# Performance work log

Measured on AMD Instinct MI355X. Metric: run time of the kernel, lower is better.

The kernel has to match this reference:

```python
import jax, jax.numpy as jnp
import numpy as np

DIM = 32
N_TOKENS = 4
HIDDEN = 2 * DIM
BATCH = 262144
EPS = 1e-5
SCALE = 1.0 / float(np.sqrt(DIM))


def _ln(x, g, b):
    m = jnp.mean(x, axis=-1, keepdims=True)
    v = jnp.mean((x - m) ** 2, axis=-1, keepdims=True)
    return (x - m) * jax.lax.rsqrt(v + EPS) * g + b


def setup_inputs() -> dict:
    key = jax.random.key(0)
    ks = jax.random.split(key, 16)
    s = 0.02
    lin = lambda k, i, o: jax.random.normal(k, (i, o), jnp.float32) * s
    return {
        "x": jax.random.normal(ks[0], (BATCH, N_TOKENS, DIM), jnp.float32),
        "w_pe": lin(ks[1], DIM, DIM),
        "b_pe": jnp.zeros((DIM,), jnp.float32),
        "pos": jax.random.normal(ks[2], (1, N_TOKENS, DIM), jnp.float32) * s,
        "ln1_g": jnp.ones((DIM,), jnp.float32),
        "ln1_b": jnp.zeros((DIM,), jnp.float32),
        "wq": lin(ks[3], DIM, DIM), "bq": jnp.zeros((DIM,), jnp.float32),
        "wk": lin(ks[4], DIM, DIM), "bk": jnp.zeros((DIM,), jnp.float32),
        "wv": lin(ks[5], DIM, DIM), "bv": jnp.zeros((DIM,), jnp.float32),
        "wo": lin(ks[6], DIM, DIM), "bo": jnp.zeros((DIM,), jnp.float32),
        "ln2_g": jnp.ones((DIM,), jnp.float32),
        "ln2_b": jnp.zeros((DIM,), jnp.float32),
        "w1": lin(ks[7], DIM, HIDDEN), "bf1": jnp.zeros((HIDDEN,), jnp.float32),
        "w2": lin(ks[8], HIDDEN, DIM), "bf2": jnp.zeros((DIM,), jnp.float32),
    }


def reference(x, w_pe, b_pe, pos, ln1_g, ln1_b, wq, bq, wk, bk, wv, bv,
              wo, bo, ln2_g, ln2_b, w1, bf1, w2, bf2):
    # patch embed + positional embedding
    x = x @ w_pe + b_pe + pos                      # [B, T, D]
    # attention block
    xa = _ln(x, ln1_g, ln1_b)
    q = xa @ wq + bq
    k = xa @ wk + bk
    v = xa @ wv + bv
    scores = jnp.einsum("btd,bsd->bts", q, k) * SCALE  # [B, T, T]
    attn = jax.nn.softmax(scores, axis=-1)
    mixed = jnp.einsum("bts,bsd->btd", attn, v)
    x = x + mixed @ wo + bo
    # MLP block (gelu tanh approximation, matching F.gelu(approximate='tanh'))
    xb = _ln(x, ln2_g, ln2_b)
    h = jax.nn.gelu(xb @ w1 + bf1, approximate=True)   # [B, T, 2D]
    x = x + h @ w2 + bf2
    return x
```

## Files before the change

### kernel.cpp

```cpp
#include <hip/hip_runtime.h>
#include <hip/hip_bf16.h>

typedef float          f32x4  __attribute__((ext_vector_type(4)));
typedef __bf16         bf16x8 __attribute__((ext_vector_type(8)));
typedef unsigned short u16x8  __attribute__((ext_vector_type(8)));
typedef unsigned int   u32;

#define DEV static __device__ __forceinline__

static constexpr int   NT       = 65536;
static constexpr float SCALE_Q2 = 0.2550349f;

DEV unsigned short f2bf(float f) {
  return __builtin_bit_cast(unsigned short, __float2bfloat16(f));
}
DEV u32 pk2(float lo, float hi) {
  u32 r;
  asm("v_cvt_pk_bf16_f32 %0, %1, %2" : "=v"(r) : "v"(lo), "v"(hi));
  return r;
}

DEV u16x8 pack8(f32x4 a, f32x4 b) {
  uint4 q;
  q.x = pk2(a[0], a[1]); q.y = pk2(a[2], a[3]);
  q.z = pk2(b[0], b[1]); q.w = pk2(b[2], b[3]);
  return __builtin_bit_cast(u16x8, q);
}

DEV f32x4 mfma(u16x8 a, u16x8 b, f32x4 c) {
  return __builtin_amdgcn_mfma_f32_16x16x32_bf16(
      __builtin_bit_cast(bf16x8, a), __builtin_bit_cast(bf16x8, b), c, 0, 0, 0);
}
DEV void wait_lds() {
  asm volatile("s_waitcnt lgkmcnt(0)" ::: "memory");
  __builtin_amdgcn_sched_barrier(0);
}

DEV u16x8 build_frag(const float* W, int N, int k0, int col, float scale) {
  u16x8 f;
#pragma unroll
  for (int e = 0; e < 8; ++e)
    f[e] = f2bf(W[(k0 + e) * N + col] * scale);
  return f;
}
DEV u16x8 fold_frag(u16x8 f, const float* gv) {
  u16x8 o;
#pragma unroll
  for (int e = 0; e < 8; ++e) {
    union { u32 i; float v; } u; u.i = ((u32)f[e]) << 16;
    o[e] = f2bf(u.v * gv[e]);
  }
  return o;
}

DEV void conv_wr(u32* buf, int wb, f32x4 a0, f32x4 a1) {
  buf[wb + 0] = pk2(a0[0], a0[1]);
  buf[wb + 1] = pk2(a0[2], a0[3]);
  buf[wb + 8] = pk2(a1[0], a1[1]);
  buf[wb + 9] = pk2(a1[2], a1[3]);
}
DEV u16x8 conv_rd(const u32* buf, int rb) {
  return __builtin_bit_cast(u16x8, *(const uint4*)(buf + rb));
}
DEV u16x8 conv_std(u32* buf, int r15, int lg, f32x4 a0, f32x4 a1) {
  conv_wr(buf, r15 * 20 + 2 * lg, a0, a1);
  wait_lds();
  return conv_rd(buf, r15 * 20 + 4 * lg);
}

DEV void ln_stats(f32x4 a, f32x4 b, float& rs, float& nm) {
  float s1 = 0.f, s2 = 0.f;
#pragma unroll
  for (int i = 0; i < 4; ++i) { s1 += a[i]; s2 = fmaf(a[i], a[i], s2); }
#pragma unroll
  for (int i = 0; i < 4; ++i) { s1 += b[i]; s2 = fmaf(b[i], b[i], s2); }
  s1 += __shfl_xor(s1, 16); s2 += __shfl_xor(s2, 16);
  s1 += __shfl_xor(s1, 32); s2 += __shfl_xor(s2, 32);
  const float m   = s1 * 0.03125f;
  const float var = fmaf(s2, 0.03125f, -m * m);
  rs = __builtin_amdgcn_rsqf(var + 1e-5f);
  nm = -m * rs;
}

DEV float gelu_t(float u) {
  const float z = u * fmaf(u * u, 0.1029428f, 2.3022083f);
  const float e = __builtin_amdgcn_exp2f(z);
  return fmaf(-u, __builtin_amdgcn_rcpf(e + 1.0f), u);
}

__global__ __launch_bounds__(256) void vit_fused(
    const float* __restrict__ x,
    const float* __restrict__ wpe, const float* __restrict__ bpe,
    const float* __restrict__ pos,
    const float* __restrict__ ln1g, const float* __restrict__ ln1b,
    const float* __restrict__ wq, const float* __restrict__ bq,
    const float* __restrict__ wk, const float* __restrict__ bk,
    const float* __restrict__ wv, const float* __restrict__ bv,
    const float* __restrict__ wo, const float* __restrict__ bo,
    const float* __restrict__ ln2g, const float* __restrict__ ln2b,
    const float* __restrict__ w1, const float* __restrict__ bf1,
    const float* __restrict__ w2, const float* __restrict__ bf2,
    float* __restrict__ out) {
  const int tid = (int)threadIdx.x;
  const int wid = tid >> 6;
  const int l   = tid & 63;
  const int r15 = l & 15;
  const int lg  = l >> 4;
  const int tk  = l & 3;

  __shared__ alignas(16) u32   s_conv[4][2][320];
  __shared__ alignas(16) float s_vh[4][576];
  u32*   bufA = s_conv[wid][0];
  u32*   bufB = s_conv[wid][1];
  float* vS   = s_vh[wid];
  u32*   vStg = (u32*)s_vh[wid];
  u32*   hB   = (u32*)s_vh[wid];

  float g1v[8], g2v[8];
#pragma unroll
  for (int e = 0; e < 8; ++e) { g1v[e] = ln1g[8 * lg + e]; g2v[e] = ln2g[8 * lg + e]; }
  const u16x8 b1f = pack8(*(const f32x4*)(ln1b + 8 * lg), *(const f32x4*)(ln1b + 8 * lg + 4));
  const u16x8 b2f = pack8(*(const f32x4*)(ln2b + 8 * lg), *(const f32x4*)(ln2b + 8 * lg + 4));

  u16x8 wpeF[2], wqF[2], wkF[2], wvF[2], woF[2], w1F[4], w2F[2][2];
  f32x4 comboC[2], bqC[2], bkC[2], bvC[2], boC[2], bf2C[2], bf1C[4];

#pragma unroll
  for (int H = 0; H < 2; ++H) {
    const int dc  = 16 * H + 4 * lg;
    const int col = 16 * H + r15;
    wpeF[H]   = build_frag(wpe, 32, 8 * lg, col, 1.f);
    woF[H]    = build_frag(wo,  32, 8 * lg, col, 1.f);
    w2F[0][H] = build_frag(w2,  32, 8 * lg,      col, 1.f);
    w2F[1][H] = build_frag(w2,  32, 32 + 8 * lg, col, 1.f);
    f32x4 cq, ck, cv, cmb, cbo, cb2;
#pragma unroll
    for (int i = 0; i < 4; ++i) {
      const int d = dc + i;
      cmb[i] = bpe[d] + pos[tk * 32 + d];
      cq[i]  = SCALE_Q2 * bq[d];
      ck[i]  = bk[d];
      cv[i]  = bv[d];
      cbo[i] = bo[d];
      cb2[i] = bf2[d];
    }
    comboC[H] = cmb; boC[H] = cbo; bf2C[H] = cb2;
    const u16x8 rq = build_frag(wq, 32, 8 * lg, col, SCALE_Q2);
    const u16x8 rk = build_frag(wk, 32, 8 * lg, col, 1.f);
    const u16x8 rv = build_frag(wv, 32, 8 * lg, col, 1.f);
    bqC[H] = mfma(rq, b1f, cq);
    bkC[H] = mfma(rk, b1f, ck);
    bvC[H] = mfma(rv, b1f, cv);
    wqF[H] = fold_frag(rq, g1v);
    wkF[H] = fold_frag(rk, g1v);
    wvF[H] = fold_frag(rv, g1v);
  }
#pragma unroll
  for (int Hp = 0; Hp < 4; ++Hp) {
    const int col = 16 * Hp + r15;
    const u16x8 r1 = build_frag(w1, 64, 8 * lg, col, 1.f);
    f32x4 c1;
#pragma unroll
    for (int i = 0; i < 4; ++i) c1[i] = bf1[16 * Hp + 4 * lg + i];
    bf1C[Hp] = mfma(r1, b2f, c1);
    w1F[Hp]  = fold_frag(r1, g2v);
  }

  const f32x4 zero4 = {0.f, 0.f, 0.f, 0.f};
  const int stride = (int)(gridDim.x << 2);
  int tile = (int)(blockIdx.x << 2) | wid;

  const float* xp = x + (size_t)(tile * 16 + r15) * 32 + 8 * lg;
  f32x4 xv0 = *(const f32x4*)(xp);
  f32x4 xv1 = *(const f32x4*)(xp + 4);
  for (; tile < NT; tile += stride) {
    const int nxt = tile + stride;
    f32x4 nx0 = xv0, nx1 = xv1;
    if (nxt < NT) {
      const float* np_ = x + (size_t)(nxt * 16 + r15) * 32 + 8 * lg;
      nx0 = *(const f32x4*)(np_);
      nx1 = *(const f32x4*)(np_ + 4);
    }
    const u16x8 xf = pack8(xv0, xv1);

    f32x4 x1a = mfma(wpeF[0], xf, comboC[0]);
    f32x4 x1b = mfma(wpeF[1], xf, comboC[1]);

    float rs, nm;
    ln_stats(x1a, x1b, rs, nm);
    f32x4 ya, yb;
#pragma unroll
    for (int i = 0; i < 4; ++i) { ya[i] = fmaf(x1a[i], rs, nm); yb[i] = fmaf(x1b[i], rs, nm); }
    const u16x8 xaf = conv_std(bufA, r15, lg, ya, yb);

    const f32x4 qa0 = mfma(wqF[0], xaf, bqC[0]);
    const f32x4 qa1 = mfma(wqF[1], xaf, bqC[1]);
    const f32x4 ka0 = mfma(wkF[0], xaf, bkC[0]);
    const f32x4 ka1 = mfma(wkF[1], xaf, bkC[1]);
    const f32x4 va0 = mfma(wvF[0], xaf, bvC[0]);
    const f32x4 va1 = mfma(wvF[1], xaf, bvC[1]);

    const int wb = r15 * 20 + 2 * lg;
    conv_wr(bufB, wb, qa0, qa1);
    conv_wr(bufA, wb, ka0, ka1);
    conv_wr(vStg, wb, va0, va1);
    wait_lds();
    const int rb = r15 * 20 + 4 * lg;
    const u16x8 qf = conv_rd(bufB, rb);
    const u16x8 kf = conv_rd(bufA, rb);
    const u16x8 vf = conv_rd(vStg, rb);

    const f32x4 vo0 = mfma(woF[0], vf, boC[0]);
    const f32x4 vo1 = mfma(woF[1], vf, boC[1]);

    const f32x4 sc = mfma(kf, qf, zero4);
    const float mx = fmaxf(fmaxf(sc[0], sc[1]), fmaxf(sc[2], sc[3]));
    const float e0 = __builtin_amdgcn_exp2f(sc[0] - mx);
    const float e1 = __builtin_amdgcn_exp2f(sc[1] - mx);
    const float e2 = __builtin_amdgcn_exp2f(sc[2] - mx);
    const float e3 = __builtin_amdgcn_exp2f(sc[3] - mx);
    const float rc = __builtin_amdgcn_rcpf((e0 + e1) + (e2 + e3));

    *(f32x4*)(vS + r15 * 36 + 4 * lg)      = vo0;
    *(f32x4*)(vS + r15 * 36 + 16 + 4 * lg) = vo1;

    const int srcb = (16 * (r15 >> 2) + r15) << 2;
    f32x4 atv;
    atv[0] = __builtin_bit_cast(float, __builtin_amdgcn_ds_bpermute(srcb, __builtin_bit_cast(int, e0 * rc)));
    atv[1] = __builtin_bit_cast(float, __builtin_amdgcn_ds_bpermute(srcb, __builtin_bit_cast(int, e1 * rc)));
    atv[2] = __builtin_bit_cast(float, __builtin_amdgcn_ds_bpermute(srcb, __builtin_bit_cast(int, e2 * rc)));
    atv[3] = __builtin_bit_cast(float, __builtin_amdgcn_ds_bpermute(srcb, __builtin_bit_cast(int, e3 * rc)));
    wait_lds();

    f32x4 m0 = zero4, m1 = zero4;
#pragma unroll
    for (int j = 0; j < 4; ++j) {
      const f32x4 v0 = *(const f32x4*)(vS + ((r15 & 12) + j) * 36 + 4 * lg);
      const f32x4 v1 = *(const f32x4*)(vS + ((r15 & 12) + j) * 36 + 16 + 4 * lg);
      m0 += atv[j] * v0;
      m1 += atv[j] * v1;
    }
    const f32x4 x2a = x1a + m0;
    const f32x4 x2b = x1b + m1;

    ln_stats(x2a, x2b, rs, nm);
#pragma unroll
    for (int i = 0; i < 4; ++i) { ya[i] = fmaf(x2a[i], rs, nm); yb[i] = fmaf(x2b[i], rs, nm); }
    const u16x8 xbf = conv_std(bufA, r15, lg, ya, yb);

#pragma unroll
    for (int Hp = 0; Hp < 4; ++Hp) {
      const f32x4 h = mfma(w1F[Hp], xbf, bf1C[Hp]);
      const int hb = r15 * 36 + 8 * Hp + 2 * lg;
      hB[hb]     = pk2(gelu_t(h[0]), gelu_t(h[1]));
      hB[hb + 1] = pk2(gelu_t(h[2]), gelu_t(h[3]));
    }
    wait_lds();
    const u16x8 hf0 = __builtin_bit_cast(u16x8, *(const uint4*)(hB + r15 * 36 + 4 * lg));
    const u16x8 hf1 = __builtin_bit_cast(u16x8, *(const uint4*)(hB + r15 * 36 + 16 + 4 * lg));

    f32x4 o0 = x2a + bf2C[0];
    f32x4 o1 = x2b + bf2C[1];
    o0 = mfma(w2F[0][0], hf0, o0);
    o0 = mfma(w2F[1][0], hf1, o0);
    o1 = mfma(w2F[0][1], hf0, o1);
    o1 = mfma(w2F[1][1], hf1, o1);

    float* op = out + (size_t)(tile * 16 + r15) * 32;
    *(f32x4*)(op + 4 * lg)      = o0;
    *(f32x4*)(op + 16 + 4 * lg) = o1;

    xv0 = nx0; xv1 = nx1;
  }
}

extern "C" void kernel_launch(void* const* d_in, const int* in_sizes, int n_in,
                              void* d_out, int out_size, void* d_ws, size_t ws_size,
                              hipStream_t stream) {
  (void)in_sizes; (void)n_in; (void)d_ws; (void)ws_size; (void)out_size;
  const float* x    = (const float*)d_in[0];
  const float* wpe  = (const float*)d_in[1];
  const float* bpe  = (const float*)d_in[2];
  const float* pos  = (const float*)d_in[3];
  const float* ln1g = (const float*)d_in[4];
  const float* ln1b = (const float*)d_in[5];
  const float* wq   = (const float*)d_in[6];
  const float* bq   = (const float*)d_in[7];
  const float* wk   = (const float*)d_in[8];
  const float* bk   = (const float*)d_in[9];
  const float* wv   = (const float*)d_in[10];
  const float* bv   = (const float*)d_in[11];
  const float* wo   = (const float*)d_in[12];
  const float* bo   = (const float*)d_in[13];
  const float* ln2g = (const float*)d_in[14];
  const float* ln2b = (const float*)d_in[15];
  const float* w1   = (const float*)d_in[16];
  const float* bf1  = (const float*)d_in[17];
  const float* w2   = (const float*)d_in[18];
  const float* bf2  = (const float*)d_in[19];

  vit_fused<<<1024, 256, 0, stream>>>(x, wpe, bpe, pos, ln1g, ln1b, wq, bq, wk, bk,
                                      wv, bv, wo, bo, ln2g, ln2b, w1, bf1, w2, bf2,
                                      (float*)d_out);
}
```

Baseline: 81.71 us.

## Stage weight MFMA fragments in shared memory instead of registers

Moves the 18 bf16 weight fragments out of per-thread registers into a shared LDS table built once by wave 0. Each tile iteration reloads them from LDS just before use, folded into the existing lgkmcnt waits. This lowers VGPR pressure so more waves can be resident and hide latency, at the cost of extra LDS read traffic every tile and a block-wide barrier at startup.

```diff
diff --git a/kernel.cpp b/kernel.cpp
--- a/kernel.cpp
+++ b/kernel.cpp
@@ -36,6 +36,12 @@
   __builtin_amdgcn_sched_barrier(0);
 }
 
+DEV u16x8 ldfrag(const u32* base, int idx, int l) {
+  int off = (idx * 64 + l) * 4;
+  asm volatile("" : "+v"(off));
+  return __builtin_bit_cast(u16x8, *(const uint4*)(base + off));
+}
+
 DEV u16x8 build_frag(const float* W, int N, int k0, int col, float scale) {
   u16x8 f;
 #pragma unroll
@@ -61,11 +67,6 @@
 }
 DEV u16x8 conv_rd(const u32* buf, int rb) {
   return __builtin_bit_cast(u16x8, *(const uint4*)(buf + rb));
-}
-DEV u16x8 conv_std(u32* buf, int r15, int lg, f32x4 a0, f32x4 a1) {
-  conv_wr(buf, r15 * 20 + 2 * lg, a0, a1);
-  wait_lds();
-  return conv_rd(buf, r15 * 20 + 4 * lg);
 }
 
 DEV void ln_stats(f32x4 a, f32x4 b, float& rs, float& nm) {
@@ -110,11 +111,13 @@
 
   __shared__ alignas(16) u32   s_conv[4][2][320];
   __shared__ alignas(16) float s_vh[4][576];
+  __shared__ alignas(16) u32   s_wf[18 * 64 * 4];
   u32*   bufA = s_conv[wid][0];
   u32*   bufB = s_conv[wid][1];
   float* vS   = s_vh[wid];
   u32*   vStg = (u32*)s_vh[wid];
   u32*   hB   = (u32*)s_vh[wid];
+  const u32* wf = s_wf;
 
   float g1v[8], g2v[8];
 #pragma unroll
@@ -122,17 +125,12 @@
   const u16x8 b1f = pack8(*(const f32x4*)(ln1b + 8 * lg), *(const f32x4*)(ln1b + 8 * lg + 4));
   const u16x8 b2f = pack8(*(const f32x4*)(ln2b + 8 * lg), *(const f32x4*)(ln2b + 8 * lg + 4));
 
-  u16x8 wpeF[2], wqF[2], wkF[2], wvF[2], woF[2], w1F[4], w2F[2][2];
   f32x4 comboC[2], bqC[2], bkC[2], bvC[2], boC[2], bf2C[2], bf1C[4];
 
 #pragma unroll
   for (int H = 0; H < 2; ++H) {
     const int dc  = 16 * H + 4 * lg;
     const int col = 16 * H + r15;
-    wpeF[H]   = build_frag(wpe, 32, 8 * lg, col, 1.f);
-    woF[H]    = build_frag(wo,  32, 8 * lg, col, 1.f);
-    w2F[0][H] = build_frag(w2,  32, 8 * lg,      col, 1.f);
-    w2F[1][H] = build_frag(w2,  32, 32 + 8 * lg, col, 1.f);
     f32x4 cq, ck, cv, cmb, cbo, cb2;
 #pragma unroll
     for (int i = 0; i < 4; ++i) {
@@ -151,9 +149,15 @@
     bqC[H] = mfma(rq, b1f, cq);
     bkC[H] = mfma(rk, b1f, ck);
     bvC[H] = mfma(rv, b1f, cv);
-    wqF[H] = fold_frag(rq, g1v);
-    wkF[H] = fold_frag(rk, g1v);
-    wvF[H] = fold_frag(rv, g1v);
+    if (wid == 0) {
+      *(uint4*)&s_wf[((0 + H) * 64 + l) * 4]  = __builtin_bit_cast(uint4, build_frag(wpe, 32, 8 * lg, col, 1.f));
+      *(uint4*)&s_wf[((2 + H) * 64 + l) * 4]  = __builtin_bit_cast(uint4, fold_frag(rq, g1v));
+      *(uint4*)&s_wf[((4 + H) * 64 + l) * 4]  = __builtin_bit_cast(uint4, fold_frag(rk, g1v));
+      *(uint4*)&s_wf[((6 + H) * 64 + l) * 4]  = __builtin_bit_cast(uint4, fold_frag(rv, g1v));
+      *(uint4*)&s_wf[((8 + H) * 64 + l) * 4]  = __builtin_bit_cast(uint4, build_frag(wo, 32, 8 * lg, col, 1.f));
+      *(uint4*)&s_wf[((14 + H) * 64 + l) * 4] = __builtin_bit_cast(uint4, build_frag(w2, 32, 8 * lg,      col, 1.f));
+      *(uint4*)&s_wf[((16 + H) * 64 + l) * 4] = __builtin_bit_cast(uint4, build_frag(w2, 32, 32 + 8 * lg, col, 1.f));
+    }
   }
 #pragma unroll
   for (int Hp = 0; Hp < 4; ++Hp) {
@@ -163,8 +167,10 @@
 #pragma unroll
     for (int i = 0; i < 4; ++i) c1[i] = bf1[16 * Hp + 4 * lg + i];
     bf1C[Hp] = mfma(r1, b2f, c1);
-    w1F[Hp]  = fold_frag(r1, g2v);
+    if (wid == 0)
+      *(uint4*)&s_wf[((10 + Hp) * 64 + l) * 4] = __builtin_bit_cast(uint4, fold_frag(r1, g2v));
   }
+  __syncthreads();
 
   const f32x4 zero4 = {0.f, 0.f, 0.f, 0.f};
   const int stride = (int)(gridDim.x << 2);
@@ -173,6 +179,10 @@
   const float* xp = x + (size_t)(tile * 16 + r15) * 32 + 8 * lg;
   f32x4 xv0 = *(const f32x4*)(xp);
   f32x4 xv1 = *(const f32x4*)(xp + 4);
+
+  u16x8 fpe0 = ldfrag(wf, 0, l), fpe1 = ldfrag(wf, 1, l);
+  wait_lds();
+
   for (; tile < NT; tile += stride) {
     const int nxt = tile + stride;
     f32x4 nx0 = xv0, nx1 = xv1;
@@ -183,36 +193,39 @@
     }
     const u16x8 xf = pack8(xv0, xv1);
 
-    f32x4 x1a = mfma(wpeF[0], xf, comboC[0]);
-    f32x4 x1b = mfma(wpeF[1], xf, comboC[1]);
-
+    f32x4 x1a = mfma(fpe0, xf, comboC[0]);
+    f32x4 x1b = mfma(fpe1, xf, comboC[1]);
     float rs, nm;
     ln_stats(x1a, x1b, rs, nm);
     f32x4 ya, yb;
 #pragma unroll
     for (int i = 0; i < 4; ++i) { ya[i] = fmaf(x1a[i], rs, nm); yb[i] = fmaf(x1b[i], rs, nm); }
-    const u16x8 xaf = conv_std(bufA, r15, lg, ya, yb);
-
-    const f32x4 qa0 = mfma(wqF[0], xaf, bqC[0]);
-    const f32x4 qa1 = mfma(wqF[1], xaf, bqC[1]);
-    const f32x4 ka0 = mfma(wkF[0], xaf, bkC[0]);
-    const f32x4 ka1 = mfma(wkF[1], xaf, bkC[1]);
-    const f32x4 va0 = mfma(wvF[0], xaf, bvC[0]);
-    const f32x4 va1 = mfma(wvF[1], xaf, bvC[1]);
-
     const int wb = r15 * 20 + 2 * lg;
+    const int rb = r15 * 20 + 4 * lg;
+    conv_wr(bufA, wb, ya, yb);
+    const u16x8 fq0 = ldfrag(wf, 2, l), fq1 = ldfrag(wf, 3, l);
+    const u16x8 fk0 = ldfrag(wf, 4, l), fk1 = ldfrag(wf, 5, l);
+    const u16x8 fv0 = ldfrag(wf, 6, l), fv1 = ldfrag(wf, 7, l);
+    wait_lds();
+
+    const u16x8 xaf = conv_rd(bufA, rb);
+    const f32x4 qa0 = mfma(fq0, xaf, bqC[0]);
+    const f32x4 qa1 = mfma(fq1, xaf, bqC[1]);
+    const f32x4 ka0 = mfma(fk0, xaf, bkC[0]);
+    const f32x4 ka1 = mfma(fk1, xaf, bkC[1]);
+    const f32x4 va0 = mfma(fv0, xaf, bvC[0]);
+    const f32x4 va1 = mfma(fv1, xaf, bvC[1]);
     conv_wr(bufB, wb, qa0, qa1);
     conv_wr(bufA, wb, ka0, ka1);
     conv_wr(vStg, wb, va0, va1);
-    wait_lds();
-    const int rb = r15 * 20 + 4 * lg;
+    const u16x8 fo0 = ldfrag(wf, 8, l), fo1 = ldfrag(wf, 9, l);
+    wait_lds();
+
     const u16x8 qf = conv_rd(bufB, rb);
     const u16x8 kf = conv_rd(bufA, rb);
     const u16x8 vf = conv_rd(vStg, rb);
-
-    const f32x4 vo0 = mfma(woF[0], vf, boC[0]);
-    const f32x4 vo1 = mfma(woF[1], vf, boC[1]);
-
+    const f32x4 vo0 = mfma(fo0, vf, boC[0]);
+    const f32x4 vo1 = mfma(fo1, vf, boC[1]);
     const f32x4 sc = mfma(kf, qf, zero4);
     const float mx = fmaxf(fmaxf(sc[0], sc[1]), fmaxf(sc[2], sc[3]));
     const float e0 = __builtin_amdgcn_exp2f(sc[0] - mx);
@@ -220,10 +233,8 @@
     const float e2 = __builtin_amdgcn_exp2f(sc[2] - mx);
     const float e3 = __builtin_amdgcn_exp2f(sc[3] - mx);
     const float rc = __builtin_amdgcn_rcpf((e0 + e1) + (e2 + e3));
-
     *(f32x4*)(vS + r15 * 36 + 4 * lg)      = vo0;
     *(f32x4*)(vS + r15 * 36 + 16 + 4 * lg) = vo1;
-
     const int srcb = (16 * (r15 >> 2) + r15) << 2;
     f32x4 atv;
     atv[0] = __builtin_bit_cast(float, __builtin_amdgcn_ds_bpermute(srcb, __builtin_bit_cast(int, e0 * rc)));
@@ -242,29 +253,52 @@
     }
     const f32x4 x2a = x1a + m0;
     const f32x4 x2b = x1b + m1;
-
     ln_stats(x2a, x2b, rs, nm);
 #pragma unroll
     for (int i = 0; i < 4; ++i) { ya[i] = fmaf(x2a[i], rs, nm); yb[i] = fmaf(x2b[i], rs, nm); }
-    const u16x8 xbf = conv_std(bufA, r15, lg, ya, yb);
-
-#pragma unroll
-    for (int Hp = 0; Hp < 4; ++Hp) {
-      const f32x4 h = mfma(w1F[Hp], xbf, bf1C[Hp]);
-      const int hb = r15 * 36 + 8 * Hp + 2 * lg;
+    conv_wr(bufA, wb, ya, yb);
+    const u16x8 f10 = ldfrag(wf, 10, l), f11 = ldfrag(wf, 11, l);
+    const u16x8 f12 = ldfrag(wf, 12, l), f13 = ldfrag(wf, 13, l);
+    wait_lds();
+
+    const u16x8 xbf = conv_rd(bufA, rb);
+    {
+      const f32x4 h = mfma(f10, xbf, bf1C[0]);
+      const int hb = r15 * 36 + 2 * lg;
       hB[hb]     = pk2(gelu_t(h[0]), gelu_t(h[1]));
       hB[hb + 1] = pk2(gelu_t(h[2]), gelu_t(h[3]));
     }
-    wait_lds();
+    {
+      const f32x4 h = mfma(f11, xbf, bf1C[1]);
+      const int hb = r15 * 36 + 8 + 2 * lg;
+      hB[hb]     = pk2(gelu_t(h[0]), gelu_t(h[1]));
+      hB[hb + 1] = pk2(gelu_t(h[2]), gelu_t(h[3]));
+    }
+    {
+      const f32x4 h = mfma(f12, xbf, bf1C[2]);
+      const int hb = r15 * 36 + 16 + 2 * lg;
+      hB[hb]     = pk2(gelu_t(h[0]), gelu_t(h[1]));
+      hB[hb + 1] = pk2(gelu_t(h[2]), gelu_t(h[3]));
+    }
+    {
+      const f32x4 h = mfma(f13, xbf, bf1C[3]);
+      const int hb = r15 * 36 + 24 + 2 * lg;
+      hB[hb]     = pk2(gelu_t(h[0]), gelu_t(h[1]));
+      hB[hb + 1] = pk2(gelu_t(h[2]), gelu_t(h[3]));
+    }
+    const u16x8 f20 = ldfrag(wf, 14, l), f21 = ldfrag(wf, 15, l);
+    const u16x8 f22 = ldfrag(wf, 16, l), f23 = ldfrag(wf, 17, l);
+    fpe0 = ldfrag(wf, 0, l); fpe1 = ldfrag(wf, 1, l);
+    wait_lds();
+
     const u16x8 hf0 = __builtin_bit_cast(u16x8, *(const uint4*)(hB + r15 * 36 + 4 * lg));
     const u16x8 hf1 = __builtin_bit_cast(u16x8, *(const uint4*)(hB + r15 * 36 + 16 + 4 * lg));
-
     f32x4 o0 = x2a + bf2C[0];
     f32x4 o1 = x2b + bf2C[1];
-    o0 = mfma(w2F[0][0], hf0, o0);
-    o0 = mfma(w2F[1][0], hf1, o0);
-    o1 = mfma(w2F[0][1], hf0, o1);
-    o1 = mfma(w2F[1][1], hf1, o1);
+    o0 = mfma(f20, hf0, o0);
+    o0 = mfma(f22, hf1, o0);
+    o1 = mfma(f21, hf0, o1);
+    o1 = mfma(f23, hf1, o1);
 
     float* op = out + (size_t)(tile * 16 + r15) * 32;
     *(f32x4*)(op + 4 * lg)      = o0;
```

Result: slower. 90.95 us (+11.3%).

## Interleave two independent tiles per wave iteration to hide LDS and MFMA latency

Applied to the files above, without the earlier changes.

Each wave now processes two tiles per loop iteration, one from each half of the batch, with every stage run for both tiles before a single shared LDS wait. This gives twice the independent work between the LDS round-trips and MFMA dependency chains, so fewer wait points stall the wave. In exchange the kernel uses double the per-wave LDS buffers and roughly twice the live registers, which may reduce occupancy.

```diff
diff --git a/kernel.cpp b/kernel.cpp
--- a/kernel.cpp
+++ b/kernel.cpp
@@ -9,6 +9,7 @@
 #define DEV static __device__ __forceinline__
 
 static constexpr int   NT       = 65536;
+static constexpr int   HALF     = NT / 2;
 static constexpr float SCALE_Q2 = 0.2550349f;
 
 DEV unsigned short f2bf(float f) {
@@ -61,11 +62,6 @@
 }
 DEV u16x8 conv_rd(const u32* buf, int rb) {
   return __builtin_bit_cast(u16x8, *(const uint4*)(buf + rb));
-}
-DEV u16x8 conv_std(u32* buf, int r15, int lg, f32x4 a0, f32x4 a1) {
-  conv_wr(buf, r15 * 20 + 2 * lg, a0, a1);
-  wait_lds();
-  return conv_rd(buf, r15 * 20 + 4 * lg);
 }
 
 DEV void ln_stats(f32x4 a, f32x4 b, float& rs, float& nm) {
@@ -108,13 +104,12 @@
   const int lg  = l >> 4;
   const int tk  = l & 3;
 
-  __shared__ alignas(16) u32   s_conv[4][2][320];
-  __shared__ alignas(16) float s_vh[4][576];
-  u32*   bufA = s_conv[wid][0];
-  u32*   bufB = s_conv[wid][1];
-  float* vS   = s_vh[wid];
-  u32*   vStg = (u32*)s_vh[wid];
-  u32*   hB   = (u32*)s_vh[wid];
+  __shared__ alignas(16) u32   s_conv[4][2][2][320];
+  __shared__ alignas(16) float s_vh[4][2][576];
+  u32*   cA[2] = { s_conv[wid][0][0], s_conv[wid][1][0] };
+  u32*   cB[2] = { s_conv[wid][0][1], s_conv[wid][1][1] };
+  float* vSf[2] = { s_vh[wid][0], s_vh[wid][1] };
+  u32*   vSu[2] = { (u32*)s_vh[wid][0], (u32*)s_vh[wid][1] };
 
   float g1v[8], g2v[8];
 #pragma unroll
@@ -170,107 +165,137 @@
   const int stride = (int)(gridDim.x << 2);
   int tile = (int)(blockIdx.x << 2) | wid;
 
-  const float* xp = x + (size_t)(tile * 16 + r15) * 32 + 8 * lg;
-  f32x4 xv0 = *(const f32x4*)(xp);
-  f32x4 xv1 = *(const f32x4*)(xp + 4);
-  for (; tile < NT; tile += stride) {
+  const int xrow = r15 * 32 + 8 * lg;
+  const int orow = r15 * 32 + 4 * lg;
+  f32x4 px0[2], px1[2];
+  {
+    const float* pa = x + (size_t)tile * 512 + xrow;
+    const float* pb = x + (size_t)(tile + HALF) * 512 + xrow;
+    px0[0] = *(const f32x4*)pa;       px1[0] = *(const f32x4*)(pa + 4);
+    px0[1] = *(const f32x4*)pb;       px1[1] = *(const f32x4*)(pb + 4);
+  }
+
+  for (; tile < HALF; tile += stride) {
     const int nxt = tile + stride;
-    f32x4 nx0 = xv0, nx1 = xv1;
-    if (nxt < NT) {
-      const float* np_ = x + (size_t)(nxt * 16 + r15) * 32 + 8 * lg;
-      nx0 = *(const f32x4*)(np_);
-      nx1 = *(const f32x4*)(np_ + 4);
-    }
-    const u16x8 xf = pack8(xv0, xv1);
-
-    f32x4 x1a = mfma(wpeF[0], xf, comboC[0]);
-    f32x4 x1b = mfma(wpeF[1], xf, comboC[1]);
-
-    float rs, nm;
-    ln_stats(x1a, x1b, rs, nm);
-    f32x4 ya, yb;
-#pragma unroll
-    for (int i = 0; i < 4; ++i) { ya[i] = fmaf(x1a[i], rs, nm); yb[i] = fmaf(x1b[i], rs, nm); }
-    const u16x8 xaf = conv_std(bufA, r15, lg, ya, yb);
-
-    const f32x4 qa0 = mfma(wqF[0], xaf, bqC[0]);
-    const f32x4 qa1 = mfma(wqF[1], xaf, bqC[1]);
-    const f32x4 ka0 = mfma(wkF[0], xaf, bkC[0]);
-    const f32x4 ka1 = mfma(wkF[1], xaf, bkC[1]);
-    const f32x4 va0 = mfma(wvF[0], xaf, bvC[0]);
-    const f32x4 va1 = mfma(wvF[1], xaf, bvC[1]);
-
+    f32x4 nx0[2] = {px0[0], px0[1]}, nx1[2] = {px1[0], px1[1]};
+    if (nxt < HALF) {
+      const float* pa = x + (size_t)nxt * 512 + xrow;
+      const float* pb = x + (size_t)(nxt + HALF) * 512 + xrow;
+      nx0[0] = *(const f32x4*)pa;     nx1[0] = *(const f32x4*)(pa + 4);
+      nx0[1] = *(const f32x4*)pb;     nx1[1] = *(const f32x4*)(pb + 4);
+    }
     const int wb = r15 * 20 + 2 * lg;
-    conv_wr(bufB, wb, qa0, qa1);
-    conv_wr(bufA, wb, ka0, ka1);
-    conv_wr(vStg, wb, va0, va1);
-    wait_lds();
     const int rb = r15 * 20 + 4 * lg;
-    const u16x8 qf = conv_rd(bufB, rb);
-    const u16x8 kf = conv_rd(bufA, rb);
-    const u16x8 vf = conv_rd(vStg, rb);
-
-    const f32x4 vo0 = mfma(woF[0], vf, boC[0]);
-    const f32x4 vo1 = mfma(woF[1], vf, boC[1]);
-
-    const f32x4 sc = mfma(kf, qf, zero4);
-    const float mx = fmaxf(fmaxf(sc[0], sc[1]), fmaxf(sc[2], sc[3]));
-    const float e0 = __builtin_amdgcn_exp2f(sc[0] - mx);
-    const float e1 = __builtin_amdgcn_exp2f(sc[1] - mx);
-    const float e2 = __builtin_amdgcn_exp2f(sc[2] - mx);
-    const float e3 = __builtin_amdgcn_exp2f(sc[3] - mx);
-    const float rc = __builtin_amdgcn_rcpf((e0 + e1) + (e2 + e3));
-
-    *(f32x4*)(vS + r15 * 36 + 4 * lg)      = vo0;
-    *(f32x4*)(vS + r15 * 36 + 16 + 4 * lg) = vo1;
-
-    const int srcb = (16 * (r15 >> 2) + r15) << 2;
-    f32x4 atv;
-    atv[0] = __builtin_bit_cast(float, __builtin_amdgcn_ds_bpermute(srcb, __builtin_bit_cast(int, e0 * rc)));
-    atv[1] = __builtin_bit_cast(float, __builtin_amdgcn_ds_bpermute(srcb, __builtin_bit_cast(int, e1 * rc)));
-    atv[2] = __builtin_bit_cast(float, __builtin_amdgcn_ds_bpermute(srcb, __builtin_bit_cast(int, e2 * rc)));
-    atv[3] = __builtin_bit_cast(float, __builtin_amdgcn_ds_bpermute(srcb, __builtin_bit_cast(int, e3 * rc)));
-    wait_lds();
-
-    f32x4 m0 = zero4, m1 = zero4;
-#pragma unroll
-    for (int j = 0; j < 4; ++j) {
-      const f32x4 v0 = *(const f32x4*)(vS + ((r15 & 12) + j) * 36 + 4 * lg);
-      const f32x4 v1 = *(const f32x4*)(vS + ((r15 & 12) + j) * 36 + 16 + 4 * lg);
-      m0 += atv[j] * v0;
-      m1 += atv[j] * v1;
-    }
-    const f32x4 x2a = x1a + m0;
-    const f32x4 x2b = x1b + m1;
-
-    ln_stats(x2a, x2b, rs, nm);
-#pragma unroll
-    for (int i = 0; i < 4; ++i) { ya[i] = fmaf(x2a[i], rs, nm); yb[i] = fmaf(x2b[i], rs, nm); }
-    const u16x8 xbf = conv_std(bufA, r15, lg, ya, yb);
-
-#pragma unroll
-    for (int Hp = 0; Hp < 4; ++Hp) {
-      const f32x4 h = mfma(w1F[Hp], xbf, bf1C[Hp]);
-      const int hb = r15 * 36 + 8 * Hp + 2 * lg;
-      hB[hb]     = pk2(gelu_t(h[0]), gelu_t(h[1]));
-      hB[hb + 1] = pk2(gelu_t(h[2]), gelu_t(h[3]));
-    }
-    wait_lds();
-    const u16x8 hf0 = __builtin_bit_cast(u16x8, *(const uint4*)(hB + r15 * 36 + 4 * lg));
-    const u16x8 hf1 = __builtin_bit_cast(u16x8, *(const uint4*)(hB + r15 * 36 + 16 + 4 * lg));
-
-    f32x4 o0 = x2a + bf2C[0];
-    f32x4 o1 = x2b + bf2C[1];
-    o0 = mfma(w2F[0][0], hf0, o0);
-    o0 = mfma(w2F[1][0], hf1, o0);
-    o1 = mfma(w2F[0][1], hf0, o1);
-    o1 = mfma(w2F[1][1], hf1, o1);
-
-    float* op = out + (size_t)(tile * 16 + r15) * 32;
-    *(f32x4*)(op + 4 * lg)      = o0;
-    *(f32x4*)(op + 16 + 4 * lg) = o1;
-
-    xv0 = nx0; xv1 = nx1;
+
+    f32x4 x1a[2], x1b[2];
+#pragma unroll
+    for (int t = 0; t < 2; ++t) {
+      const u16x8 xf = pack8(px0[t], px1[t]);
+      x1a[t] = mfma(wpeF[0], xf, comboC[0]);
+      x1b[t] = mfma(wpeF[1], xf, comboC[1]);
+      float rs, nm;
+      ln_stats(x1a[t], x1b[t], rs, nm);
+      f32x4 ya, yb;
+#pragma unroll
+      for (int i = 0; i < 4; ++i) { ya[i] = fmaf(x1a[t][i], rs, nm); yb[i] = fmaf(x1b[t][i], rs, nm); }
+      conv_wr(cA[t], wb, ya, yb);
+    }
+    wait_lds();
+
+#pragma unroll
+    for (int t = 0; t < 2; ++t) {
+      const u16x8 xaf = conv_rd(cA[t], rb);
+      const f32x4 qa0 = mfma(wqF[0], xaf, bqC[0]);
+      const f32x4 qa1 = mfma(wqF[1], xaf, bqC[1]);
+      const f32x4 ka0 = mfma(wkF[0], xaf, bkC[0]);
+      const f32x4 ka1 = mfma(wkF[1], xaf, bkC[1]);
+      const f32x4 va0 = mfma(wvF[0], xaf, bvC[0]);
+      const f32x4 va1 = mfma(wvF[1], xaf, bvC[1]);
+      conv_wr(cB[t], wb, qa0, qa1);
+      conv_wr(cA[t], wb, ka0, ka1);
+      conv_wr(vSu[t], wb, va0, va1);
+    }
+    wait_lds();
+
+    f32x4 atv[2];
+#pragma unroll
+    for (int t = 0; t < 2; ++t) {
+      const u16x8 qf = conv_rd(cB[t], rb);
+      const u16x8 kf = conv_rd(cA[t], rb);
+      const u16x8 vf = conv_rd(vSu[t], rb);
+      const f32x4 vo0 = mfma(woF[0], vf, boC[0]);
+      const f32x4 vo1 = mfma(woF[1], vf, boC[1]);
+      const f32x4 sc  = mfma(kf, qf, zero4);
+      const float mx = fmaxf(fmaxf(sc[0], sc[1]), fmaxf(sc[2], sc[3]));
+      const float e0 = __builtin_amdgcn_exp2f(sc[0] - mx);
+      const float e1 = __builtin_amdgcn_exp2f(sc[1] - mx);
+      const float e2 = __builtin_amdgcn_exp2f(sc[2] - mx);
+      const float e3 = __builtin_amdgcn_exp2f(sc[3] - mx);
+      const float rc = __builtin_amdgcn_rcpf((e0 + e1) + (e2 + e3));
+      *(f32x4*)(vSf[t] + r15 * 36 + 4 * lg)      = vo0;
+      *(f32x4*)(vSf[t] + r15 * 36 + 16 + 4 * lg) = vo1;
+      const int srcb = (16 * (r15 >> 2) + r15) << 2;
+      atv[t][0] = __builtin_bit_cast(float, __builtin_amdgcn_ds_bpermute(srcb, __builtin_bit_cast(int, e0 * rc)));
+      atv[t][1] = __builtin_bit_cast(float, __builtin_amdgcn_ds_bpermute(srcb, __builtin_bit_cast(int, e1 * rc)));
+      atv[t][2] = __builtin_bit_cast(float, __builtin_amdgcn_ds_bpermute(srcb, __builtin_bit_cast(int, e2 * rc)));
+      atv[t][3] = __builtin_bit_cast(float, __builtin_amdgcn_ds_bpermute(srcb, __builtin_bit_cast(int, e3 * rc)));
+    }
+    wait_lds();
+
+    f32x4 x2a[2], x2b[2];
+#pragma unroll
+    for (int t = 0; t < 2; ++t) {
+      f32x4 m0 = zero4, m1 = zero4;
+#pragma unroll
+      for (int j = 0; j < 4; ++j) {
+        const f32x4 v0 = *(const f32x4*)(vSf[t] + ((r15 & 12) + j) * 36 + 4 * lg);
+        const f32x4 v1 = *(const f32x4*)(vSf[t] + ((r15 & 12) + j) * 36 + 16 + 4 * lg);
+        m0 += atv[t][j] * v0;
+        m1 += atv[t][j] * v1;
+      }
+      x2a[t] = x1a[t] + m0;
+      x2b[t] = x1b[t] + m1;
+      float rs, nm;
+      ln_stats(x2a[t], x2b[t], rs, nm);
+      f32x4 ya, yb;
+#pragma unroll
+      for (int i = 0; i < 4; ++i) { ya[i] = fmaf(x2a[t][i], rs, nm); yb[i] = fmaf(x2b[t][i], rs, nm); }
+      conv_wr(cA[t], wb, ya, yb);
+    }
+    wait_lds();
+
+#pragma unroll
+    for (int t = 0; t < 2; ++t) {
+      const u16x8 xbf = conv_rd(cA[t], rb);
+      u32* hB = vSu[t];
+#pragma unroll
+      for (int Hp = 0; Hp < 4; ++Hp) {
+        const f32x4 h = mfma(w1F[Hp], xbf, bf1C[Hp]);
+        const int hb = r15 * 36 + 8 * Hp + 2 * lg;
+        hB[hb]     = pk2(gelu_t(h[0]), gelu_t(h[1]));
+        hB[hb + 1] = pk2(gelu_t(h[2]), gelu_t(h[3]));
+      }
+    }
+    wait_lds();
+
+#pragma unroll
+    for (int t = 0; t < 2; ++t) {
+      const u32* hB = vSu[t];
+      const u16x8 hf0 = __builtin_bit_cast(u16x8, *(const uint4*)(hB + r15 * 36 + 4 * lg));
+      const u16x8 hf1 = __builtin_bit_cast(u16x8, *(const uint4*)(hB + r15 * 36 + 16 + 4 * lg));
+      f32x4 o0 = x2a[t] + bf2C[0];
+      f32x4 o1 = x2b[t] + bf2C[1];
+      o0 = mfma(w2F[0][0], hf0, o0);
+      o0 = mfma(w2F[1][0], hf1, o0);
+      o1 = mfma(w2F[0][1], hf0, o1);
+      o1 = mfma(w2F[1][1], hf1, o1);
+      float* op = out + (size_t)(tile + t * HALF) * 512 + orow;
+      *(f32x4*)(op)      = o0;
+      *(f32x4*)(op + 16) = o1;
+    }
+
+    px0[0] = nx0[0]; px1[0] = nx1[0];
+    px0[1] = nx0[1]; px1[1] = nx1[1];
   }
 }
 
```

Result: no change. 80.55 us (-1.4%).

## Stage weight fragments in LDS, reorder Wo projection, raise occupancy

Applied to the files above, without the earlier changes.

Moves the patch-embed and W2 weight fragments out of registers into a shared LDS buffer. Each wave reloads them per tile, which cuts register pressure so the kernel can run at three blocks per SM under launch bounds. The attention output projection is now applied after mixing (attn·V then Wo) rather than projecting V first, which needs an extra LDS conversion. The grid shrinks to 768 blocks to match the higher occupancy. The cost is extra LDS reads per tile and one block-wide sync at setup.

```diff
diff --git a/kernel.cpp b/kernel.cpp
--- a/kernel.cpp
+++ b/kernel.cpp
@@ -36,6 +36,12 @@
   __builtin_amdgcn_sched_barrier(0);
 }
 
+DEV u16x8 ldfrag(const u32* base, int idx, int l) {
+  int off = (idx * 64 + l) * 4;
+  asm volatile("" : "+v"(off));
+  return __builtin_bit_cast(u16x8, *(const uint4*)(base + off));
+}
+
 DEV u16x8 build_frag(const float* W, int N, int k0, int col, float scale) {
   u16x8 f;
 #pragma unroll
@@ -66,6 +72,17 @@
   conv_wr(buf, r15 * 20 + 2 * lg, a0, a1);
   wait_lds();
   return conv_rd(buf, r15 * 20 + 4 * lg);
+}
+DEV void conv_qk(u32* bq_, u32* bk_, int r15, int lg,
+                 f32x4 q0, f32x4 q1, f32x4 k0, f32x4 k1,
+                 u16x8& qf, u16x8& kf) {
+  const int wb = r15 * 20 + 2 * lg;
+  conv_wr(bq_, wb, q0, q1);
+  conv_wr(bk_, wb, k0, k1);
+  wait_lds();
+  const int rb = r15 * 20 + 4 * lg;
+  qf = conv_rd(bq_, rb);
+  kf = conv_rd(bk_, rb);
 }
 
 DEV void ln_stats(f32x4 a, f32x4 b, float& rs, float& nm) {
@@ -88,7 +105,7 @@
   return fmaf(-u, __builtin_amdgcn_rcpf(e + 1.0f), u);
 }
 
-__global__ __launch_bounds__(256) void vit_fused(
+__global__ __launch_bounds__(256, 3) void vit_fused(
     const float* __restrict__ x,
     const float* __restrict__ wpe, const float* __restrict__ bpe,
     const float* __restrict__ pos,
@@ -110,11 +127,12 @@
 
   __shared__ alignas(16) u32   s_conv[4][2][320];
   __shared__ alignas(16) float s_vh[4][576];
+  __shared__ alignas(16) u32   s_wf[6 * 64 * 4];
   u32*   bufA = s_conv[wid][0];
   u32*   bufB = s_conv[wid][1];
   float* vS   = s_vh[wid];
-  u32*   vStg = (u32*)s_vh[wid];
   u32*   hB   = (u32*)s_vh[wid];
+  const u32* wf = s_wf;
 
   float g1v[8], g2v[8];
 #pragma unroll
@@ -122,17 +140,19 @@
   const u16x8 b1f = pack8(*(const f32x4*)(ln1b + 8 * lg), *(const f32x4*)(ln1b + 8 * lg + 4));
   const u16x8 b2f = pack8(*(const f32x4*)(ln2b + 8 * lg), *(const f32x4*)(ln2b + 8 * lg + 4));
 
-  u16x8 wpeF[2], wqF[2], wkF[2], wvF[2], woF[2], w1F[4], w2F[2][2];
+  u16x8 wqF[2], wkF[2], wvF[2], woF[2], w1F[4];
   f32x4 comboC[2], bqC[2], bkC[2], bvC[2], boC[2], bf2C[2], bf1C[4];
 
 #pragma unroll
   for (int H = 0; H < 2; ++H) {
     const int dc  = 16 * H + 4 * lg;
     const int col = 16 * H + r15;
-    wpeF[H]   = build_frag(wpe, 32, 8 * lg, col, 1.f);
-    woF[H]    = build_frag(wo,  32, 8 * lg, col, 1.f);
-    w2F[0][H] = build_frag(w2,  32, 8 * lg,      col, 1.f);
-    w2F[1][H] = build_frag(w2,  32, 32 + 8 * lg, col, 1.f);
+    woF[H] = build_frag(wo, 32, 8 * lg, col, 1.f);
+    if (wid == 0) {
+      *(uint4*)&s_wf[((0 + H) * 64 + l) * 4] = __builtin_bit_cast(uint4, build_frag(wpe, 32, 8 * lg, col, 1.f));
+      *(uint4*)&s_wf[((2 + H) * 64 + l) * 4] = __builtin_bit_cast(uint4, build_frag(w2, 32, 8 * lg,      col, 1.f));
+      *(uint4*)&s_wf[((4 + H) * 64 + l) * 4] = __builtin_bit_cast(uint4, build_frag(w2, 32, 32 + 8 * lg, col, 1.f));
+    }
     f32x4 cq, ck, cv, cmb, cbo, cb2;
 #pragma unroll
     for (int i = 0; i < 4; ++i) {
@@ -165,6 +185,7 @@
     bf1C[Hp] = mfma(r1, b2f, c1);
     w1F[Hp]  = fold_frag(r1, g2v);
   }
+  __syncthreads();
 
   const f32x4 zero4 = {0.f, 0.f, 0.f, 0.f};
   const int stride = (int)(gridDim.x << 2);
@@ -173,6 +194,8 @@
   const float* xp = x + (size_t)(tile * 16 + r15) * 32 + 8 * lg;
   f32x4 xv0 = *(const f32x4*)(xp);
   f32x4 xv1 = *(const f32x4*)(xp + 4);
+  u16x8 fpe0 = ldfrag(wf, 0, l), fpe1 = ldfrag(wf, 1, l);
+
   for (; tile < NT; tile += stride) {
     const int nxt = tile + stride;
     f32x4 nx0 = xv0, nx1 = xv1;
@@ -183,8 +206,8 @@
     }
     const u16x8 xf = pack8(xv0, xv1);
 
-    f32x4 x1a = mfma(wpeF[0], xf, comboC[0]);
-    f32x4 x1b = mfma(wpeF[1], xf, comboC[1]);
+    f32x4 x1a = mfma(fpe0, xf, comboC[0]);
+    f32x4 x1b = mfma(fpe1, xf, comboC[1]);
 
     float rs, nm;
     ln_stats(x1a, x1b, rs, nm);
@@ -200,52 +223,45 @@
     const f32x4 va0 = mfma(wvF[0], xaf, bvC[0]);
     const f32x4 va1 = mfma(wvF[1], xaf, bvC[1]);
 
-    const int wb = r15 * 20 + 2 * lg;
-    conv_wr(bufB, wb, qa0, qa1);
-    conv_wr(bufA, wb, ka0, ka1);
-    conv_wr(vStg, wb, va0, va1);
-    wait_lds();
-    const int rb = r15 * 20 + 4 * lg;
-    const u16x8 qf = conv_rd(bufB, rb);
-    const u16x8 kf = conv_rd(bufA, rb);
-    const u16x8 vf = conv_rd(vStg, rb);
-
-    const f32x4 vo0 = mfma(woF[0], vf, boC[0]);
-    const f32x4 vo1 = mfma(woF[1], vf, boC[1]);
+    *(f32x4*)(vS + r15 * 36 + 4 * lg)      = va0;
+    *(f32x4*)(vS + r15 * 36 + 16 + 4 * lg) = va1;
+
+    u16x8 qf, kf;
+    conv_qk(bufB, bufA, r15, lg, qa0, qa1, ka0, ka1, qf, kf);
 
     const f32x4 sc = mfma(kf, qf, zero4);
-    const float mx = fmaxf(fmaxf(sc[0], sc[1]), fmaxf(sc[2], sc[3]));
-    const float e0 = __builtin_amdgcn_exp2f(sc[0] - mx);
-    const float e1 = __builtin_amdgcn_exp2f(sc[1] - mx);
-    const float e2 = __builtin_amdgcn_exp2f(sc[2] - mx);
-    const float e3 = __builtin_amdgcn_exp2f(sc[3] - mx);
-    const float rc = __builtin_amdgcn_rcpf((e0 + e1) + (e2 + e3));
-
-    *(f32x4*)(vS + r15 * 36 + 4 * lg)      = vo0;
-    *(f32x4*)(vS + r15 * 36 + 16 + 4 * lg) = vo1;
-
-    const int srcb = (16 * (r15 >> 2) + r15) << 2;
-    f32x4 atv;
-    atv[0] = __builtin_bit_cast(float, __builtin_amdgcn_ds_bpermute(srcb, __builtin_bit_cast(int, e0 * rc)));
-    atv[1] = __builtin_bit_cast(float, __builtin_amdgcn_ds_bpermute(srcb, __builtin_bit_cast(int, e1 * rc)));
-    atv[2] = __builtin_bit_cast(float, __builtin_amdgcn_ds_bpermute(srcb, __builtin_bit_cast(int, e2 * rc)));
-    atv[3] = __builtin_bit_cast(float, __builtin_amdgcn_ds_bpermute(srcb, __builtin_bit_cast(int, e3 * rc)));
-    wait_lds();
-
-    f32x4 m0 = zero4, m1 = zero4;
-#pragma unroll
-    for (int j = 0; j < 4; ++j) {
-      const f32x4 v0 = *(const f32x4*)(vS + ((r15 & 12) + j) * 36 + 4 * lg);
-      const f32x4 v1 = *(const f32x4*)(vS + ((r15 & 12) + j) * 36 + 16 + 4 * lg);
-      m0 += atv[j] * v0;
-      m1 += atv[j] * v1;
-    }
-    const f32x4 x2a = x1a + m0;
-    const f32x4 x2b = x1b + m1;
-
-    ln_stats(x2a, x2b, rs, nm);
-#pragma unroll
-    for (int i = 0; i < 4; ++i) { ya[i] = fmaf(x2a[i], rs, nm); yb[i] = fmaf(x2b[i], rs, nm); }
+    {
+      const float mx = fmaxf(fmaxf(sc[0], sc[1]), fmaxf(sc[2], sc[3]));
+      const float e0 = __builtin_amdgcn_exp2f(sc[0] - mx);
+      const float e1 = __builtin_amdgcn_exp2f(sc[1] - mx);
+      const float e2 = __builtin_amdgcn_exp2f(sc[2] - mx);
+      const float e3 = __builtin_amdgcn_exp2f(sc[3] - mx);
+      const float rc = __builtin_amdgcn_rcpf((e0 + e1) + (e2 + e3));
+      f32x4 p; p[0] = e0 * rc; p[1] = e1 * rc; p[2] = e2 * rc; p[3] = e3 * rc;
+      const int srcb = (16 * (r15 >> 2) + r15) << 2;
+      f32x4 atv;
+      atv[0] = __builtin_bit_cast(float, __builtin_amdgcn_ds_bpermute(srcb, __builtin_bit_cast(int, p[0])));
+      atv[1] = __builtin_bit_cast(float, __builtin_amdgcn_ds_bpermute(srcb, __builtin_bit_cast(int, p[1])));
+      atv[2] = __builtin_bit_cast(float, __builtin_amdgcn_ds_bpermute(srcb, __builtin_bit_cast(int, p[2])));
+      atv[3] = __builtin_bit_cast(float, __builtin_amdgcn_ds_bpermute(srcb, __builtin_bit_cast(int, p[3])));
+      wait_lds();
+
+      f32x4 m0 = zero4, m1 = zero4;
+#pragma unroll
+      for (int j = 0; j < 4; ++j) {
+        const f32x4 v0 = *(const f32x4*)(vS + ((r15 & 12) + j) * 36 + 4 * lg);
+        const f32x4 v1 = *(const f32x4*)(vS + ((r15 & 12) + j) * 36 + 16 + 4 * lg);
+        m0 += atv[j] * v0;
+        m1 += atv[j] * v1;
+      }
+      const u16x8 mf = conv_std(bufB, r15, lg, m0, m1);
+      x1a = mfma(woF[0], mf, x1a) + boC[0];
+      x1b = mfma(woF[1], mf, x1b) + boC[1];
+    }
+
+    ln_stats(x1a, x1b, rs, nm);
+#pragma unroll
+    for (int i = 0; i < 4; ++i) { ya[i] = fmaf(x1a[i], rs, nm); yb[i] = fmaf(x1b[i], rs, nm); }
     const u16x8 xbf = conv_std(bufA, r15, lg, ya, yb);
 
 #pragma unroll
@@ -255,16 +271,21 @@
       hB[hb]     = pk2(gelu_t(h[0]), gelu_t(h[1]));
       hB[hb + 1] = pk2(gelu_t(h[2]), gelu_t(h[3]));
     }
+    const u16x8 f20 = ldfrag(wf, 2, l);
+    const u16x8 f21 = ldfrag(wf, 3, l);
+    const u16x8 f22 = ldfrag(wf, 4, l);
+    const u16x8 f23 = ldfrag(wf, 5, l);
+    fpe0 = ldfrag(wf, 0, l); fpe1 = ldfrag(wf, 1, l);
     wait_lds();
     const u16x8 hf0 = __builtin_bit_cast(u16x8, *(const uint4*)(hB + r15 * 36 + 4 * lg));
     const u16x8 hf1 = __builtin_bit_cast(u16x8, *(const uint4*)(hB + r15 * 36 + 16 + 4 * lg));
 
-    f32x4 o0 = x2a + bf2C[0];
-    f32x4 o1 = x2b + bf2C[1];
-    o0 = mfma(w2F[0][0], hf0, o0);
-    o0 = mfma(w2F[1][0], hf1, o0);
-    o1 = mfma(w2F[0][1], hf0, o1);
-    o1 = mfma(w2F[1][1], hf1, o1);
+    f32x4 o0 = x1a + bf2C[0];
+    f32x4 o1 = x1b + bf2C[1];
+    o0 = mfma(f20, hf0, o0);
+    o0 = mfma(f22, hf1, o0);
+    o1 = mfma(f21, hf0, o1);
+    o1 = mfma(f23, hf1, o1);
 
     float* op = out + (size_t)(tile * 16 + r15) * 32;
     *(f32x4*)(op + 4 * lg)      = o0;
@@ -299,7 +320,7 @@
   const float* w2   = (const float*)d_in[18];
   const float* bf2  = (const float*)d_in[19];
 
-  vit_fused<<<1024, 256, 0, stream>>>(x, wpe, bpe, pos, ln1g, ln1b, wq, bq, wk, bk,
-                                      wv, bv, wo, bo, ln2g, ln2b, w1, bf1, w2, bf2,
-                                      (float*)d_out);
-}
+  vit_fused<<<768, 256, 0, stream>>>(x, wpe, bpe, pos, ln1g, ln1b, wq, bq, wk, bk,
+                                     wv, bv, wo, bo, ln2g, ln2b, w1, bf1, w2, bf2,
+                                     (float*)d_out);
+}
```

New measurement: 105.0 us. 1.28x slower.
